# Kernel tuning notes

Measured on AMD Instinct MI355X. Metric: run time of the kernel, lower is better.

The kernel has to match this reference:

```python
import jax, jax.numpy as jnp
import numpy as np

N_QUBITS = 8
DEPTH = 3
FEATURE_DIM = 512
NUM_CLASSES = 10
BATCH = 8192
CDTYPE = jnp.complex64


def _ry_batched(theta):
    # theta: (B,) -> (B,2,2) real RY matrices cast to complex
    c = jnp.cos(theta / 2)
    s = jnp.sin(theta / 2)
    row0 = jnp.stack([c, -s], axis=-1)
    row1 = jnp.stack([s, c], axis=-1)
    return jnp.stack([row0, row1], axis=-2).astype(CDTYPE)


def _ry(theta):
    c = jnp.cos(theta / 2).astype(CDTYPE)
    s = jnp.sin(theta / 2).astype(CDTYPE)
    return jnp.stack([jnp.stack([c, -s]), jnp.stack([s, c])])


def _rx(theta):
    c = jnp.cos(theta / 2).astype(CDTYPE)
    js = (-1j) * jnp.sin(theta / 2).astype(CDTYPE)
    return jnp.stack([jnp.stack([c, js]), jnp.stack([js, c])])


def _apply_1q(state, U, q, n):
    # state: (B, 2,...,2) little-endian: axis (n - q) holds qubit q's bit
    ax = n - q
    sm = jnp.moveaxis(state, ax, -1)
    if U.ndim == 3:  # per-batch gate
        new = jnp.einsum('b...k,bjk->b...j', sm, U)
    else:  # shared gate
        new = jnp.einsum('...k,jk->...j', sm, U)
    return jnp.moveaxis(new, -1, ax)


def _cnot(state, c, t, n):
    ax_c = n - c
    ax_t = n - t
    s0, s1 = jnp.split(state, 2, axis=ax_c)
    s1 = jnp.flip(s1, axis=ax_t)  # X on target where control=1
    return jnp.concatenate([s0, s1], axis=ax_c)


def _quantum_expect(angles, qnn_w, n=N_QUBITS, depth=DEPTH):
    # angles: (B, n) encoding angles; qnn_w: (depth*n*3,) circuit weights
    B = angles.shape[0]
    state = jnp.zeros((B,) + (2,) * n, CDTYPE)
    state = state.at[(slice(None),) + (0,) * n].set(1.0)
    # RY encoding layer (batched angles)
    for q in range(n):
        state = _apply_1q(state, _ry_batched(angles[:, q]), q, n)
    wr = qnn_w.reshape(depth, n, 3)
    for l in range(depth):
        for q in range(n):
            state = _apply_1q(state, _rx(wr[l, q, 0]), q, n)
            state = _apply_1q(state, _ry(wr[l, q, 1]), q, n)
            state = _apply_1q(state, _rx(wr[l, q, 2]), q, n)
        for q in range(n - 1):
            state = _cnot(state, q, q + 1, n)
        state = _cnot(state, n - 1, 0, n)
    # PauliZ expectation per qubit: sum probs weighted by (+1, -1) on that qubit's axis
    p = state.real ** 2 + state.imag ** 2  # (B, 2,...,2) real
    z = jnp.array([1.0, -1.0], p.dtype)
    outs = []
    for q in range(n):
        ax = n - q
        sign = z.reshape((1,) * ax + (2,) + (1,) * q)
        outs.append(jnp.sum(p * sign, axis=tuple(range(1, n + 1))))
    return jnp.stack(outs, axis=-1)  # (B, n)


def setup_inputs() -> dict:
    key = jax.random.key(0)
    k1, k2, k3, k4, k5 = jax.random.split(key, 5)
    x = jax.random.normal(k1, (BATCH, FEATURE_DIM), jnp.float32)
    bound_p = 1.0 / np.sqrt(FEATURE_DIM)
    proj_w = jax.random.uniform(k2, (N_QUBITS, FEATURE_DIM), jnp.float32, -bound_p, bound_p)
    qnn_w = 0.01 * jax.random.normal(k3, (DEPTH * N_QUBITS * 3,), jnp.float32)
    bound_o = 1.0 / np.sqrt(N_QUBITS)
    out_w = jax.random.uniform(k4, (NUM_CLASSES, N_QUBITS), jnp.float32, -bound_o, bound_o)
    out_b = jax.random.uniform(k5, (NUM_CLASSES,), jnp.float32, -bound_o, bound_o)
    return {'x': x, 'proj_w': proj_w, 'qnn_w': qnn_w, 'out_w': out_w, 'out_b': out_b}


def reference(x, proj_w, qnn_w, out_w, out_b):
    angles = jnp.tanh(x @ proj_w.T) * (jnp.pi / 2)  # (B, n_qubits)
    q_out = _quantum_expect(angles, qnn_w)          # (B, n_qubits)
    return q_out @ out_w.T + out_b                  # (B, num_classes)
```

## Files before the change

### kernel.cpp

```cpp
#include <hip/hip_runtime.h>
#include <math.h>

#define NQ 8
#define NDEPTH 3
#define FEAT 512
#define NCLS 10
#define NBATCH 8192

typedef _Float16 v8h __attribute__((ext_vector_type(8)));
typedef _Float16 v4h __attribute__((ext_vector_type(4)));
typedef float v4f __attribute__((ext_vector_type(4)));


__global__ void precompute(const float* __restrict__ qnn_w,
                           const float* __restrict__ out_w,
                           float* __restrict__ gates, float* __restrict__ T) {
    int i = threadIdx.x;
    if (i < NDEPTH * NQ) {
        float t0 = 0.5f * qnn_w[i * 3 + 0];
        float t1 = 0.5f * qnn_w[i * 3 + 1];
        float t2 = 0.5f * qnn_w[i * 3 + 2];
        float c0 = cosf(t0), s0 = sinf(t0);
        float c1 = cosf(t1), s1 = sinf(t1);
        float c2 = cosf(t2), s2 = sinf(t2);
        float m00r =  c1 * c0, m00i =  s1 * s0;
        float m01r = -s1 * c0, m01i = -c1 * s0;
        float m10r =  s1 * c0, m10i = -c1 * s0;
        float m11r =  c1 * c0, m11i = -s1 * s0;
        float* g = gates + i * 8;
        g[0] =  c2 * m00r + s2 * m10i;  g[1] =  c2 * m00i - s2 * m10r;
        g[2] =  c2 * m01r + s2 * m11i;  g[3] =  c2 * m01i - s2 * m11r;
        g[4] =  s2 * m00i + c2 * m10r;  g[5] = -s2 * m00r + c2 * m10i;
        g[6] =  s2 * m01i + c2 * m11r;  g[7] = -s2 * m01r + c2 * m11i;
    }
    if (i < 256) {
#pragma unroll
        for (int c = 0; c < NCLS; c++) {
            float s = 0.f;
#pragma unroll
            for (int q = 0; q < NQ; q++)
                s += (((i >> q) & 1) ? -1.f : 1.f) * out_w[c * NQ + q];
            T[i * NCLS + c] = s;
        }
    }
}

template <int CTRL, int ROW_MASK>
__device__ __forceinline__ float dpp_term(float v) {
    return __int_as_float(__builtin_amdgcn_update_dpp(
        0, __float_as_int(v), CTRL, ROW_MASK, 0xf, true));
}

__device__ __forceinline__ float wave_sum_bcast(float v) {
    v += dpp_term<0x111, 0xf>(v);
    v += dpp_term<0x112, 0xf>(v);
    v += dpp_term<0x114, 0xf>(v);
    v += dpp_term<0x118, 0xf>(v);
    v += dpp_term<0x142, 0xa>(v);
    v += dpp_term<0x143, 0xc>(v);
    return __int_as_float(__builtin_amdgcn_readlane(__float_as_int(v), 63));
}

__device__ __forceinline__ float bcastlane(float v, int srclane) {
    return __int_as_float(__builtin_amdgcn_readlane(__float_as_int(v), srclane));
}

template <int CTRL>
__device__ __forceinline__ float dpp_xor(float v) {
    return __int_as_float(__builtin_amdgcn_update_dpp(
        0, __float_as_int(v), CTRL, 0xf, 0xf, true));
}

__device__ __forceinline__ float fast_tanh(float v) {
    float e = __expf(2.f * v);
    return 1.f - 2.f / (e + 1.f);
}

__device__ __forceinline__ void cgate_pair(const float* __restrict__ u,
        float& r0, float& i0, float& r1, float& i1) {
    float nr0 = u[0]*r0 - u[1]*i0 + u[2]*r1 - u[3]*i1;
    float ni0 = u[0]*i0 + u[1]*r0 + u[2]*i1 + u[3]*r1;
    float nr1 = u[4]*r0 - u[5]*i0 + u[6]*r1 - u[7]*i1;
    float ni1 = u[4]*i0 + u[5]*r0 + u[6]*i1 + u[7]*r1;
    r0 = nr0; i0 = ni0; r1 = nr1; i1 = ni1;
}

__device__ __forceinline__ void cgate_shfl(const float* __restrict__ u, int bit,
        int mask, float (&re)[4], float (&im)[4]) {
    float dr  = bit ? u[6] : u[0], di = bit ? u[7] : u[1];
    float orr = bit ? u[4] : u[2], oi = bit ? u[5] : u[3];
#pragma unroll
    for (int j = 0; j < 4; j++) {
        float pr = __shfl_xor(re[j], mask);
        float pi = __shfl_xor(im[j], mask);
        float nr = dr*re[j] - di*im[j] + orr*pr - oi*pi;
        float ni = dr*im[j] + di*re[j] + orr*pi + oi*pr;
        re[j] = nr; im[j] = ni;
    }
}

template <int CTRL>
__device__ __forceinline__ void cgate_dpp(const float* __restrict__ u, int bit,
        float (&re)[4], float (&im)[4]) {
    float dr  = bit ? u[6] : u[0], di = bit ? u[7] : u[1];
    float orr = bit ? u[4] : u[2], oi = bit ? u[5] : u[3];
#pragma unroll
    for (int j = 0; j < 4; j++) {
        float pr = dpp_xor<CTRL>(re[j]);
        float pi = dpp_xor<CTRL>(im[j]);
        float nr = dr*re[j] - di*im[j] + orr*pr - oi*pi;
        float ni = dr*im[j] + di*re[j] + orr*pi + oi*pr;
        re[j] = nr; im[j] = ni;
    }
}

__device__ __forceinline__ void apply_circuit(const float* __restrict__ gates,
        int lane, float (&re)[4], float (&im)[4]) {
#pragma unroll
    for (int l = 0; l < NDEPTH; l++) {
        const float* g = gates + l * NQ * 8;
        cgate_pair(g, re[0], im[0], re[1], im[1]);
        cgate_pair(g, re[2], im[2], re[3], im[3]);
        cgate_pair(g + 8,  re[0], im[0], re[2], im[2]);
        cgate_pair(g + 8,  re[1], im[1], re[3], im[3]);
        cgate_dpp<0xB1>(g + 16, lane & 1,        re, im);
        cgate_dpp<0x4E>(g + 24, (lane >> 1) & 1, re, im);
        cgate_shfl(g + 32, (lane >> 2) & 1, 4,  re, im);
        cgate_shfl(g + 40, (lane >> 3) & 1, 8,  re, im);
        cgate_shfl(g + 48, (lane >> 4) & 1, 16, re, im);
        cgate_shfl(g + 56, (lane >> 5) & 1, 32, re, im);
        { float t = re[1]; re[1] = re[3]; re[3] = t;
          t = im[1]; im[1] = im[3]; im[3] = t; }
        int base  = lane ^ ((lane << 1) & 63);
        int base2 = base ^ 1;
        re[0] = __shfl(re[0], base);  im[0] = __shfl(im[0], base);
        re[1] = __shfl(re[1], base);  im[1] = __shfl(im[1], base);
        re[2] = __shfl(re[2], base2); im[2] = __shfl(im[2], base2);
        re[3] = __shfl(re[3], base2); im[3] = __shfl(im[3], base2);
        int bit5 = (lane >> 5) & 1;
        {
            float t0 = bit5 ? re[1] : re[0], t1 = bit5 ? re[0] : re[1];
            float t2 = bit5 ? re[3] : re[2], t3 = bit5 ? re[2] : re[3];
            re[0] = t0; re[1] = t1; re[2] = t2; re[3] = t3;
            t0 = bit5 ? im[1] : im[0]; t1 = bit5 ? im[0] : im[1];
            t2 = bit5 ? im[3] : im[2]; t3 = bit5 ? im[2] : im[3];
            im[0] = t0; im[1] = t1; im[2] = t2; im[3] = t3;
        }
    }
}

__global__ __launch_bounds__(256) void enc_kernel(
        const float* __restrict__ x, const float* __restrict__ proj_w,
        _Float16* __restrict__ enc) {
    int tid  = threadIdx.x;
    int lane = tid & 63;
    int b    = blockIdx.x * 4 + (tid >> 6);

    const float4* xr4 = (const float4*)(x + (size_t)b * FEAT);
    float4 xa = xr4[lane], xb = xr4[lane + 64];
    float dq[8];
#pragma unroll
    for (int q = 0; q < 8; q++) {
        const float4* pw4 = (const float4*)(proj_w + q * FEAT);
        float4 wa = pw4[lane], wb = pw4[lane + 64];
        float acc = xa.x*wa.x + xa.y*wa.y + xa.z*wa.z + xa.w*wa.w
                  + xb.x*wb.x + xb.y*wb.y + xb.z*wb.z + xb.w*wb.w;
        dq[q] = wave_sum_bcast(acc);
    }
    int qsel = lane >> 3;
    float a0 = (qsel & 4) ? dq[4] : dq[0];
    float a1 = (qsel & 4) ? dq[5] : dq[1];
    float a2 = (qsel & 4) ? dq[6] : dq[2];
    float a3 = (qsel & 4) ? dq[7] : dq[3];
    float b0 = (qsel & 2) ? a2 : a0;
    float b1 = (qsel & 2) ? a3 : a1;
    float dsel = (qsel & 1) ? b1 : b0;
    float th = fast_tanh(dsel) * 0.78539816339744830962f;
    float se = __sinf(th), ce = __cosf(th);
    float cq[8], sq[8];
#pragma unroll
    for (int q = 0; q < 8; q++) {
        cq[q] = bcastlane(ce, q * 8);
        sq[q] = bcastlane(se, q * 8);
    }
    float F = 1.f;
#pragma unroll
    for (int q = 2; q < 8; q++) {
        int bit = (lane >> (q - 2)) & 1;
        F *= bit ? sq[q] : cq[q];
    }
    v4h ev;
    ev[0] = (_Float16)(F * cq[0] * cq[1]);
    ev[1] = (_Float16)(F * sq[0] * cq[1]);
    ev[2] = (_Float16)(F * cq[0] * sq[1]);
    ev[3] = (_Float16)(F * sq[0] * sq[1]);
    *(v4h*)(enc + (size_t)b * 256 + lane * 4) = ev;
}

__global__ __launch_bounds__(256) void build_w(
        const float* __restrict__ gates,
        _Float16* __restrict__ Bre, _Float16* __restrict__ Bim) {
    int tid  = threadIdx.x;
    int lane = tid & 63;
    int p    = blockIdx.x * 4 + (tid >> 6);

    float re[4], im[4];
#pragma unroll
    for (int j = 0; j < 4; j++) {
        re[j] = (lane * 4 + j == p) ? 1.f : 0.f;
        im[j] = 0.f;
    }
    apply_circuit(gates, lane, re, im);

    int t  = lane >> 2;
    int kk = p >> 5;
    int qp = (p >> 3) & 3;
    int j  = p & 7;
#pragma unroll
    for (int r = 0; r < 4; r++) {
        int n15  = (lane & 3) * 4 + r;
        int flat = ((t * 8 + kk) * 64 + qp * 16 + n15) * 8 + j;
        Bre[flat] = (_Float16)re[r];
        Bim[flat] = (_Float16)im[r];
    }
}

__global__ __launch_bounds__(64) void gemm_head(
        const _Float16* __restrict__ enc,
        const _Float16* __restrict__ Bre, const _Float16* __restrict__ Bim,
        const float* __restrict__ T, const float* __restrict__ out_b,
        float* __restrict__ out) {
    int lane = threadIdx.x;
    int rowbase = blockIdx.x * 16;
    int m = lane & 15, quad = lane >> 4;

    v8h a[8];
#pragma unroll
    for (int kk = 0; kk < 8; kk++)
        a[kk] = *(const v8h*)(enc + (size_t)(rowbase + m) * 256 + kk * 32 + quad * 8);

    float oacc[4][NCLS] = {};
#pragma unroll
    for (int t = 0; t < 16; t++) {
        int col = t * 16 + m;
        float tc[NCLS];
#pragma unroll
        for (int c = 0; c < NCLS; c++) tc[c] = T[col * NCLS + c];

        v4f ar = {0.f, 0.f, 0.f, 0.f}, ai = {0.f, 0.f, 0.f, 0.f};
#pragma unroll
        for (int kk = 0; kk < 8; kk++) {
            size_t fb = ((size_t)(t * 8 + kk)) * 512 + (size_t)lane * 8;
            v8h br = *(const v8h*)(Bre + fb);
            v8h bi = *(const v8h*)(Bim + fb);
            ar = __builtin_amdgcn_mfma_f32_16x16x32_f16(a[kk], br, ar, 0, 0, 0);
            ai = __builtin_amdgcn_mfma_f32_16x16x32_f16(a[kk], bi, ai, 0, 0, 0);
        }
#pragma unroll
        for (int r = 0; r < 4; r++) {
            float pv = ar[r] * ar[r] + ai[r] * ai[r];
#pragma unroll
            for (int c = 0; c < NCLS; c++)
                oacc[r][c] = fmaf(pv, tc[c], oacc[r][c]);
        }
    }
#pragma unroll
    for (int r = 0; r < 4; r++) {
#pragma unroll
        for (int c = 0; c < NCLS; c++) {
            float v = oacc[r][c];
            v += dpp_term<0x111, 0xf>(v);
            v += dpp_term<0x112, 0xf>(v);
            v += dpp_term<0x114, 0xf>(v);
            v += dpp_term<0x118, 0xf>(v);
            oacc[r][c] = v;
        }
    }
    if (m == 15) {
#pragma unroll
        for (int r = 0; r < 4; r++) {
            int row = rowbase + quad * 4 + r;
#pragma unroll
            for (int c = 0; c < NCLS; c++)
                out[row * NCLS + c] = oacc[r][c] + out_b[c];
        }
    }
}

extern "C" void kernel_launch(void* const* d_in, const int* in_sizes, int n_in,
                              void* d_out, int out_size, void* d_ws, size_t ws_size,
                              hipStream_t stream) {
    const float* x      = (const float*)d_in[0];
    const float* proj_w = (const float*)d_in[1];
    const float* qnn_w  = (const float*)d_in[2];
    const float* out_w  = (const float*)d_in[3];
    const float* out_b  = (const float*)d_in[4];
    float* out = (float*)d_out;

    char* ws = (char*)d_ws;
    float*     gates = (float*)(ws + 0);
    float*     T     = (float*)(ws + 4096);
    _Float16*  Bre   = (_Float16*)(ws + 16384);
    _Float16*  Bim   = (_Float16*)(ws + 16384 + 131072);
    _Float16*  enc   = (_Float16*)(ws + 278528);

    precompute<<<1, 256, 0, stream>>>(qnn_w, out_w, gates, T);
    enc_kernel<<<NBATCH / 4, 256, 0, stream>>>(x, proj_w, enc);
    build_w<<<64, 256, 0, stream>>>(gates, Bre, Bim);
    gemm_head<<<NBATCH / 16, 64, 0, stream>>>(enc, Bre, Bim, T, out_b, out);
}
```

Before: 101.3 us.

## Fuse encoding projection into GEMM head via MFMA and merge setup kernels

Replaces the four-kernel pipeline with two kernels. The precompute and circuit-matrix build now run in one kernel, with gates held in shared memory and proj_w converted to fp16. The projection x@proj_w^T moves into the GEMM kernel as an fp16 MFMA, and the product-state encoding is built in registers, so the intermediate enc buffer round-trip and two launches disappear. The fp16 conversion of x and proj_w adds precision risk, and each head block now reads x directly and stages T in LDS.

```diff
diff --git a/kernel.cpp b/kernel.cpp
--- a/kernel.cpp
+++ b/kernel.cpp
@@ -8,61 +8,13 @@
 #define NBATCH 8192
 
 typedef _Float16 v8h __attribute__((ext_vector_type(8)));
-typedef _Float16 v4h __attribute__((ext_vector_type(4)));
 typedef float v4f __attribute__((ext_vector_type(4)));
 
-
-__global__ void precompute(const float* __restrict__ qnn_w,
-                           const float* __restrict__ out_w,
-                           float* __restrict__ gates, float* __restrict__ T) {
-    int i = threadIdx.x;
-    if (i < NDEPTH * NQ) {
-        float t0 = 0.5f * qnn_w[i * 3 + 0];
-        float t1 = 0.5f * qnn_w[i * 3 + 1];
-        float t2 = 0.5f * qnn_w[i * 3 + 2];
-        float c0 = cosf(t0), s0 = sinf(t0);
-        float c1 = cosf(t1), s1 = sinf(t1);
-        float c2 = cosf(t2), s2 = sinf(t2);
-        float m00r =  c1 * c0, m00i =  s1 * s0;
-        float m01r = -s1 * c0, m01i = -c1 * s0;
-        float m10r =  s1 * c0, m10i = -c1 * s0;
-        float m11r =  c1 * c0, m11i = -s1 * s0;
-        float* g = gates + i * 8;
-        g[0] =  c2 * m00r + s2 * m10i;  g[1] =  c2 * m00i - s2 * m10r;
-        g[2] =  c2 * m01r + s2 * m11i;  g[3] =  c2 * m01i - s2 * m11r;
-        g[4] =  s2 * m00i + c2 * m10r;  g[5] = -s2 * m00r + c2 * m10i;
-        g[6] =  s2 * m01i + c2 * m11r;  g[7] = -s2 * m01r + c2 * m11i;
-    }
-    if (i < 256) {
-#pragma unroll
-        for (int c = 0; c < NCLS; c++) {
-            float s = 0.f;
-#pragma unroll
-            for (int q = 0; q < NQ; q++)
-                s += (((i >> q) & 1) ? -1.f : 1.f) * out_w[c * NQ + q];
-            T[i * NCLS + c] = s;
-        }
-    }
-}
 
 template <int CTRL, int ROW_MASK>
 __device__ __forceinline__ float dpp_term(float v) {
     return __int_as_float(__builtin_amdgcn_update_dpp(
         0, __float_as_int(v), CTRL, ROW_MASK, 0xf, true));
-}
-
-__device__ __forceinline__ float wave_sum_bcast(float v) {
-    v += dpp_term<0x111, 0xf>(v);
-    v += dpp_term<0x112, 0xf>(v);
-    v += dpp_term<0x114, 0xf>(v);
-    v += dpp_term<0x118, 0xf>(v);
-    v += dpp_term<0x142, 0xa>(v);
-    v += dpp_term<0x143, 0xc>(v);
-    return __int_as_float(__builtin_amdgcn_readlane(__float_as_int(v), 63));
-}
-
-__device__ __forceinline__ float bcastlane(float v, int srclane) {
-    return __int_as_float(__builtin_amdgcn_readlane(__float_as_int(v), srclane));
 }
 
 template <int CTRL>
@@ -149,68 +101,58 @@
     }
 }
 
-__global__ __launch_bounds__(256) void enc_kernel(
-        const float* __restrict__ x, const float* __restrict__ proj_w,
-        _Float16* __restrict__ enc) {
-    int tid  = threadIdx.x;
-    int lane = tid & 63;
-    int b    = blockIdx.x * 4 + (tid >> 6);
-
-    const float4* xr4 = (const float4*)(x + (size_t)b * FEAT);
-    float4 xa = xr4[lane], xb = xr4[lane + 64];
-    float dq[8];
-#pragma unroll
-    for (int q = 0; q < 8; q++) {
-        const float4* pw4 = (const float4*)(proj_w + q * FEAT);
-        float4 wa = pw4[lane], wb = pw4[lane + 64];
-        float acc = xa.x*wa.x + xa.y*wa.y + xa.z*wa.z + xa.w*wa.w
-                  + xb.x*wb.x + xb.y*wb.y + xb.z*wb.z + xb.w*wb.w;
-        dq[q] = wave_sum_bcast(acc);
-    }
-    int qsel = lane >> 3;
-    float a0 = (qsel & 4) ? dq[4] : dq[0];
-    float a1 = (qsel & 4) ? dq[5] : dq[1];
-    float a2 = (qsel & 4) ? dq[6] : dq[2];
-    float a3 = (qsel & 4) ? dq[7] : dq[3];
-    float b0 = (qsel & 2) ? a2 : a0;
-    float b1 = (qsel & 2) ? a3 : a1;
-    float dsel = (qsel & 1) ? b1 : b0;
-    float th = fast_tanh(dsel) * 0.78539816339744830962f;
-    float se = __sinf(th), ce = __cosf(th);
-    float cq[8], sq[8];
-#pragma unroll
-    for (int q = 0; q < 8; q++) {
-        cq[q] = bcastlane(ce, q * 8);
-        sq[q] = bcastlane(se, q * 8);
-    }
-    float F = 1.f;
-#pragma unroll
-    for (int q = 2; q < 8; q++) {
-        int bit = (lane >> (q - 2)) & 1;
-        F *= bit ? sq[q] : cq[q];
-    }
-    v4h ev;
-    ev[0] = (_Float16)(F * cq[0] * cq[1]);
-    ev[1] = (_Float16)(F * sq[0] * cq[1]);
-    ev[2] = (_Float16)(F * cq[0] * sq[1]);
-    ev[3] = (_Float16)(F * sq[0] * sq[1]);
-    *(v4h*)(enc + (size_t)b * 256 + lane * 4) = ev;
-}
-
-__global__ __launch_bounds__(256) void build_w(
-        const float* __restrict__ gates,
+__global__ __launch_bounds__(64) void build_all(
+        const float* __restrict__ qnn_w, const float* __restrict__ proj_w,
+        const float* __restrict__ out_w,
+        float* __restrict__ T, _Float16* __restrict__ PB,
         _Float16* __restrict__ Bre, _Float16* __restrict__ Bim) {
-    int tid  = threadIdx.x;
-    int lane = tid & 63;
-    int p    = blockIdx.x * 4 + (tid >> 6);
-
+    __shared__ float gl[NDEPTH * NQ * 8];
+    int tid = threadIdx.x;
+    if (tid < NDEPTH * NQ) {
+        float t0 = 0.5f * qnn_w[tid * 3 + 0];
+        float t1 = 0.5f * qnn_w[tid * 3 + 1];
+        float t2 = 0.5f * qnn_w[tid * 3 + 2];
+        float c0 = cosf(t0), s0 = sinf(t0);
+        float c1 = cosf(t1), s1 = sinf(t1);
+        float c2 = cosf(t2), s2 = sinf(t2);
+        float m00r =  c1 * c0, m00i =  s1 * s0;
+        float m01r = -s1 * c0, m01i = -c1 * s0;
+        float m10r =  s1 * c0, m10i = -c1 * s0;
+        float m11r =  c1 * c0, m11i = -s1 * s0;
+        float* g = gl + tid * 8;
+        g[0] =  c2 * m00r + s2 * m10i;  g[1] =  c2 * m00i - s2 * m10r;
+        g[2] =  c2 * m01r + s2 * m11i;  g[3] =  c2 * m01i - s2 * m11r;
+        g[4] =  s2 * m00i + c2 * m10r;  g[5] = -s2 * m00r + c2 * m10i;
+        g[6] =  s2 * m01i + c2 * m11r;  g[7] = -s2 * m01r + c2 * m11i;
+    }
+    if (blockIdx.x == 0) {
+        for (int i = tid; i < 256; i += 64) {
+#pragma unroll
+            for (int c = 0; c < NCLS; c++) {
+                float s = 0.f;
+#pragma unroll
+                for (int q = 0; q < NQ; q++)
+                    s += (((i >> q) & 1) ? -1.f : 1.f) * out_w[c * NQ + q];
+                T[i * NCLS + c] = s;
+            }
+        }
+        for (int e = 0; e < 128; e++) {
+            int idx = e * 64 + tid;
+            int n = idx >> 9, k = idx & 511;
+            PB[idx] = (n < 8) ? (_Float16)proj_w[n * FEAT + k] : (_Float16)0.f;
+        }
+    }
+    __syncthreads();
+
+    int lane = tid;
+    int p = blockIdx.x;
     float re[4], im[4];
 #pragma unroll
     for (int j = 0; j < 4; j++) {
         re[j] = (lane * 4 + j == p) ? 1.f : 0.f;
         im[j] = 0.f;
     }
-    apply_circuit(gates, lane, re, im);
+    apply_circuit(gl, lane, re, im);
 
     int t  = lane >> 2;
     int kk = p >> 5;
@@ -225,19 +167,70 @@
     }
 }
 
-__global__ __launch_bounds__(64) void gemm_head(
-        const _Float16* __restrict__ enc,
+__global__ __launch_bounds__(128) void enc_gemm_head(
+        const float* __restrict__ x, const _Float16* __restrict__ PB,
         const _Float16* __restrict__ Bre, const _Float16* __restrict__ Bim,
         const float* __restrict__ T, const float* __restrict__ out_b,
         float* __restrict__ out) {
-    int lane = threadIdx.x;
-    int rowbase = blockIdx.x * 16;
-    int m = lane & 15, quad = lane >> 4;
-
-    v8h a[8];
+    __shared__ float Tl[256 * NCLS];
+    __shared__ float cs[2][16][16];
+
+    int tid = threadIdx.x;
+    for (int e = 0; e < 20; e++) Tl[e * 128 + tid] = T[e * 128 + tid];
+    __syncthreads();
+
+    int lane = tid & 63;
+    int gw   = tid >> 6;
+    int m    = lane & 15, quad = lane >> 4;
+    int rowbase = (blockIdx.x * 2 + gw) * 16;
+
+    const float* xrow = x + (size_t)(rowbase + m) * FEAT;
+    v4f dacc = {0.f, 0.f, 0.f, 0.f};
+#pragma unroll
+    for (int kk = 0; kk < 16; kk++) {
+        int k0 = kk * 32 + quad * 8;
+        float4 xa = *(const float4*)(xrow + k0);
+        float4 xb = *(const float4*)(xrow + k0 + 4);
+        v8h av;
+        av[0] = (_Float16)xa.x; av[1] = (_Float16)xa.y;
+        av[2] = (_Float16)xa.z; av[3] = (_Float16)xa.w;
+        av[4] = (_Float16)xb.x; av[5] = (_Float16)xb.y;
+        av[6] = (_Float16)xb.z; av[7] = (_Float16)xb.w;
+        v8h bv = *(const v8h*)(PB + m * FEAT + k0);
+        dacc = __builtin_amdgcn_mfma_f32_16x16x32_f16(av, bv, dacc, 0, 0, 0);
+    }
+#pragma unroll
+    for (int r = 0; r < 4; r++) {
+        float th = fast_tanh(dacc[r]) * 0.78539816339744830962f;
+        float sv = __sinf(th), cv = __cosf(th);
+        if (m < 8) {
+            cs[gw][quad * 4 + r][m * 2]     = cv;
+            cs[gw][quad * 4 + r][m * 2 + 1] = sv;
+        }
+    }
+    float cq[8], sq[8];
+#pragma unroll
+    for (int q = 0; q < 8; q++) {
+        cq[q] = cs[gw][m][q * 2];
+        sq[q] = cs[gw][m][q * 2 + 1];
+    }
+
+    float t01[4] = {cq[0]*cq[1], sq[0]*cq[1], cq[0]*sq[1], sq[0]*sq[1]};
+    float plow[8];
+#pragma unroll
+    for (int j = 0; j < 8; j++) plow[j] = t01[j & 3] * ((j & 4) ? sq[2] : cq[2]);
+    float pqd = ((quad & 1) ? sq[3] : cq[3]) * ((quad & 2) ? sq[4] : cq[4]);
+    float t56[4] = {cq[5]*cq[6], sq[5]*cq[6], cq[5]*sq[6], sq[5]*sq[6]};
+    float phi[8];
 #pragma unroll
     for (int kk = 0; kk < 8; kk++)
-        a[kk] = *(const v8h*)(enc + (size_t)(rowbase + m) * 256 + kk * 32 + quad * 8);
+        phi[kk] = t56[kk & 3] * ((kk & 4) ? sq[7] : cq[7]) * pqd;
+    v8h aenc[8];
+#pragma unroll
+    for (int kk = 0; kk < 8; kk++)
+#pragma unroll
+        for (int j = 0; j < 8; j++)
+            aenc[kk][j] = (_Float16)(plow[j] * phi[kk]);
 
     float oacc[4][NCLS] = {};
 #pragma unroll
@@ -245,7 +238,7 @@
         int col = t * 16 + m;
         float tc[NCLS];
 #pragma unroll
-        for (int c = 0; c < NCLS; c++) tc[c] = T[col * NCLS + c];
+        for (int c = 0; c < NCLS; c++) tc[c] = Tl[col * NCLS + c];
 
         v4f ar = {0.f, 0.f, 0.f, 0.f}, ai = {0.f, 0.f, 0.f, 0.f};
 #pragma unroll
@@ -253,8 +246,8 @@
             size_t fb = ((size_t)(t * 8 + kk)) * 512 + (size_t)lane * 8;
             v8h br = *(const v8h*)(Bre + fb);
             v8h bi = *(const v8h*)(Bim + fb);
-            ar = __builtin_amdgcn_mfma_f32_16x16x32_f16(a[kk], br, ar, 0, 0, 0);
-            ai = __builtin_amdgcn_mfma_f32_16x16x32_f16(a[kk], bi, ai, 0, 0, 0);
+            ar = __builtin_amdgcn_mfma_f32_16x16x32_f16(aenc[kk], br, ar, 0, 0, 0);
+            ai = __builtin_amdgcn_mfma_f32_16x16x32_f16(aenc[kk], bi, ai, 0, 0, 0);
         }
 #pragma unroll
         for (int r = 0; r < 4; r++) {
@@ -298,14 +291,11 @@
     float* out = (float*)d_out;
 
     char* ws = (char*)d_ws;
-    float*     gates = (float*)(ws + 0);
-    float*     T     = (float*)(ws + 4096);
-    _Float16*  Bre   = (_Float16*)(ws + 16384);
-    _Float16*  Bim   = (_Float16*)(ws + 16384 + 131072);
-    _Float16*  enc   = (_Float16*)(ws + 278528);
-
-    precompute<<<1, 256, 0, stream>>>(qnn_w, out_w, gates, T);
-    enc_kernel<<<NBATCH / 4, 256, 0, stream>>>(x, proj_w, enc);
-    build_w<<<64, 256, 0, stream>>>(gates, Bre, Bim);
-    gemm_head<<<NBATCH / 16, 64, 0, stream>>>(enc, Bre, Bim, T, out_b, out);
-}
+    float*    T   = (float*)(ws + 0);
+    _Float16* PB  = (_Float16*)(ws + 16384);
+    _Float16* Bre = (_Float16*)(ws + 32768);
+    _Float16* Bim = (_Float16*)(ws + 163840);
+
+    build_all<<<256, 64, 0, stream>>>(qnn_w, proj_w, out_w, T, PB, Bre, Bim);
+    enc_gemm_head<<<NBATCH / 32, 128, 0, stream>>>(x, PB, Bre, Bim, T, out_b, out);
+}
```

After: 115.5 us. 1.14x slower.
